# Performance work log

Hardware: AMD Instinct MI355X
Metric: run time of the kernel (lower is better)

Reference implementation:

```python
import jax, jax.numpy as jnp
import numpy as np

B, T, D, E, C = 4, 4096, 2048, 8, 1024
H = D // E  # per-expert hidden = out_features // num_experts = 256


def setup_inputs() -> dict:
    key = jax.random.key(0)
    ks = jax.random.split(key, 7)
    x = jax.random.normal(ks[0], (B, T, D), dtype=jnp.float32)
    # nn.Linear-style init scale ~ 1/sqrt(fan_in)
    W1 = jax.random.normal(ks[1], (E, H, D), dtype=jnp.float32) / np.sqrt(D)
    b1 = jax.random.normal(ks[2], (E, H), dtype=jnp.float32) / np.sqrt(D)
    W2 = jax.random.normal(ks[3], (E, D, H), dtype=jnp.float32) / np.sqrt(D)
    b2 = jax.random.normal(ks[4], (D,), dtype=jnp.float32) / np.sqrt(D)
    expert_indices = jax.random.randint(ks[5], (B, E, C), 0, T, dtype=jnp.int32)
    expert_gate = jax.random.uniform(ks[6], (B, E, C), dtype=jnp.float32)
    return {"x": x, "W1": W1, "b1": b1, "W2": W2, "b2": b2,
            "expert_indices": expert_indices, "expert_gate": expert_gate,
            "num_tokens": T}


def reference(x, W1, b1, W2, b2, expert_indices, expert_gate, num_tokens):
    # x: (B,T,D); expert_indices/expert_gate: (B,E,C)
    Bb = x.shape[0]
    Ee, Cc = expert_indices.shape[1], expert_indices.shape[2]
    b_idx = jnp.arange(Bb)[:, None, None]
    # dispatch: gather tokens per expert -> (B,E,C,D)
    sel = x[b_idx, expert_indices]
    # contract: per-expert GEMM -> (B,E,C,H)
    h = jnp.einsum('becd,ehd->bech', sel, W1) + b1[None, :, None, :]
    h = jax.nn.gelu(h, approximate=False)
    # expand: per-expert GEMM -> (B,E,C,D), shared output bias
    y = jnp.einsum('bech,eoh->beco', h, W2) + b2
    y = y * expert_gate[..., None]
    # combine: gated scatter-add back to token positions -> (B,T,D)
    out = jnp.zeros((Bb, num_tokens, x.shape[2]), dtype=x.dtype)
    out = out.at[jnp.arange(Bb)[:, None], expert_indices.reshape(Bb, Ee * Cc)].add(
        y.reshape(Bb, Ee * Cc, -1))
    return out
```

## Files before the change

### kernel.cpp

```cpp
#include <hip/hip_runtime.h>
#include <hip/hip_bf16.h>
#include <math.h>

#define B_ 4
#define T_ 4096
#define D_ 2048
#define E_ 8
#define C_ 1024
#define H_ 256
#define SLOTCAP 32

typedef unsigned short u16;
typedef unsigned long long u64;
typedef __attribute__((ext_vector_type(8))) short short8;
typedef __attribute__((ext_vector_type(4))) float f32x4;

__device__ __forceinline__ u16 f2bf_n(float f) {
    union { __hip_bfloat16 b; u16 u; } v;
    v.b = __float2bfloat16(f);
    return v.u;
}
__device__ __forceinline__ float bf2f(u16 u) {
    union { unsigned u; float f; } v; v.u = ((unsigned)u) << 16;
    return v.f;
}

__device__ __forceinline__ int swz(int row, int chunk) {
    return (row << 6) + ((chunk ^ (row & 7)) << 3);
}

__device__ __forceinline__ void gload16(const void* g, void* l) {
    __builtin_amdgcn_global_load_lds(
        (const __attribute__((address_space(1))) void*)g,
        (__attribute__((address_space(3))) void*)l, 16, 0, 0);
}

__global__ __launch_bounds__(256) void conv_x_bf16(
    const float* __restrict__ src, u16* __restrict__ dst, int n)
{
    int i = (blockIdx.x * 256 + threadIdx.x) * 4;
    if (i >= n) return;
    f32x4 v = *reinterpret_cast<const f32x4*>(src + i);
    u16 o[4];
    o[0] = f2bf_n(v[0]); o[1] = f2bf_n(v[1]); o[2] = f2bf_n(v[2]); o[3] = f2bf_n(v[3]);
    *reinterpret_cast<u64*>(dst + i) = *reinterpret_cast<const u64*>(o);
}

__global__ __launch_bounds__(256) void conv_w1_img(
    const float* __restrict__ W1, u16* __restrict__ img)
{
    const int cid = blockIdx.x * 256 + threadIdx.x;
    const int e = cid >> 16;
    const int kt = (cid >> 11) & 31;
    const int row = (cid >> 3) & 255;
    const int sc = cid & 7;
    const float* s = W1 + (((size_t)e * 256 + row) * 2048 + kt * 64
                           + ((sc ^ (row & 7)) << 3));
    f32x4 v0 = *reinterpret_cast<const f32x4*>(s);
    f32x4 v1 = *reinterpret_cast<const f32x4*>(s + 4);
    u16 o[8];
    #pragma unroll
    for (int j = 0; j < 4; ++j) { o[j] = f2bf_n(v0[j]); o[j + 4] = f2bf_n(v1[j]); }
    *reinterpret_cast<short8*>(img + (size_t)cid * 8) =
        *reinterpret_cast<const short8*>(o);
}

__global__ __launch_bounds__(256) void conv_w2_img(
    const float* __restrict__ W2, u16* __restrict__ img)
{
    const int cid = blockIdx.x * 256 + threadIdx.x;
    const int e = cid >> 16;
    const int nt = (cid >> 13) & 7;
    const int kt = (cid >> 11) & 3;
    const int row = (cid >> 3) & 255;
    const int sc = cid & 7;
    const float* s = W2 + (((size_t)e * 2048 + nt * 256 + row) * 256 + kt * 64
                           + ((sc ^ (row & 7)) << 3));
    f32x4 v0 = *reinterpret_cast<const f32x4*>(s);
    f32x4 v1 = *reinterpret_cast<const f32x4*>(s + 4);
    u16 o[8];
    #pragma unroll
    for (int j = 0; j < 4; ++j) { o[j] = f2bf_n(v0[j]); o[j + 4] = f2bf_n(v1[j]); }
    *reinterpret_cast<short8*>(img + (size_t)cid * 8) =
        *reinterpret_cast<const short8*>(o);
}

__global__ __launch_bounds__(512) void gemm1_v6(
    const u16* __restrict__ xbf, const u16* __restrict__ W1img,
    const float* __restrict__ b1, const int* __restrict__ idx,
    u16* __restrict__ Himg)
{
    const int mt = blockIdx.x;
    const int be = blockIdx.y;
    const int b = be >> 3, e = be & 7;
    const int m0 = mt * 128;

    __shared__ __align__(16) u16 As[2][8192];
    __shared__ __align__(16) u16 Bs[2][16384];
    __shared__ int toks[128];
    __shared__ float bs1[256];

    const int tid = threadIdx.x;
    if (tid < 128) toks[tid] = idx[(b * E_ + e) * C_ + m0 + tid];
    if (tid < 256) bs1[tid] = b1[e * H_ + tid];
    __syncthreads();

    const int lane = tid & 63, wid = tid >> 6;
    const int wm = wid >> 2, wn = wid & 3;
    const int l15 = lane & 15, lk = lane >> 4;

    const int s0 = tid;
    const int arow0 = s0 >> 3, asc = s0 & 7;
    const int arow1 = arow0 + 64;
    const u16* aSrc0 = xbf + ((size_t)b * T_ + toks[arow0]) * D_
                           + ((asc ^ (arow0 & 7)) << 3);
    const u16* aSrc1 = xbf + ((size_t)b * T_ + toks[arow1]) * D_
                           + ((asc ^ (arow1 & 7)) << 3);
    const u16* bSrc = W1img + (size_t)e * 32 * 16384 + (size_t)s0 * 8;
    const int ldsb = wid * 512;

#define G1_ISSUE(buf, kt)                                                     \
    do {                                                                      \
        const u16* b_ = bSrc + (size_t)(kt) * 16384;                          \
        gload16(aSrc0 + (kt) * 64, &As[buf][ldsb]);                           \
        gload16(aSrc1 + (kt) * 64, &As[buf][4096 + ldsb]);                    \
        gload16(b_,                &Bs[buf][ldsb]);                           \
        gload16(b_ + 4096,         &Bs[buf][4096 + ldsb]);                    \
        gload16(b_ + 8192,         &Bs[buf][8192 + ldsb]);                    \
        gload16(b_ + 12288,        &Bs[buf][12288 + ldsb]);                   \
    } while (0)

    f32x4 acc[4][4];
    #pragma unroll
    for (int i = 0; i < 4; ++i)
        #pragma unroll
        for (int j = 0; j < 4; ++j)
            acc[i][j] = (f32x4){0.f, 0.f, 0.f, 0.f};

    G1_ISSUE(0, 0);
    G1_ISSUE(1, 1);

    const int NT = D_ / 64;
    for (int t = 0; t < NT; ++t) {
        const int cur = t & 1;
        if (t < NT - 1) asm volatile("s_waitcnt vmcnt(6)" ::: "memory");
        else            asm volatile("s_waitcnt vmcnt(0)" ::: "memory");
        __builtin_amdgcn_s_barrier();
        __builtin_amdgcn_sched_barrier(0);
        #pragma unroll
        for (int kk = 0; kk < 2; ++kk) {
            short8 af[4], bfr[4];
            #pragma unroll
            for (int m = 0; m < 4; ++m) {
                const int row = wm * 64 + m * 16 + l15;
                af[m] = *reinterpret_cast<const short8*>(
                    &As[cur][swz(row, kk * 4 + lk)]);
            }
            #pragma unroll
            for (int n = 0; n < 4; ++n) {
                const int row = wn * 64 + n * 16 + l15;
                bfr[n] = *reinterpret_cast<const short8*>(
                    &Bs[cur][swz(row, kk * 4 + lk)]);
            }
            __builtin_amdgcn_s_setprio(1);
            #pragma unroll
            for (int m = 0; m < 4; ++m)
                #pragma unroll
                for (int n = 0; n < 4; ++n)
                    acc[m][n] = __builtin_amdgcn_mfma_f32_16x16x32_bf16(
                        bfr[n], af[m], acc[m][n], 0, 0, 0);
            __builtin_amdgcn_s_setprio(0);
        }
        asm volatile("s_waitcnt lgkmcnt(0)" ::: "memory");
        __builtin_amdgcn_s_barrier();
        __builtin_amdgcn_sched_barrier(0);
        if (t + 2 < NT) G1_ISSUE(cur, t + 2);
    }
#undef G1_ISSUE

    const size_t hblk = ((size_t)(be * 8 + mt) * 4 + wn) * 8192;
    #pragma unroll
    for (int m = 0; m < 4; ++m) {
        const int row = wm * 64 + m * 16 + l15;
        #pragma unroll
        for (int n = 0; n < 4; ++n) {
            const int hb = wn * 64 + n * 16 + lk * 4;
            u16 o[4];
            #pragma unroll
            for (int r = 0; r < 4; ++r) {
                float h = acc[m][n][r] + bs1[hb + r];
                float g = 0.5f * h * (1.0f + erff(h * 0.70710678118f));
                o[r] = f2bf_n(g);
            }
            const int lc = (n * 2 + (lk >> 1)) ^ (row & 7);
            u16* p = Himg + hblk + row * 64 + lc * 8 + (lk & 1) * 4;
            *reinterpret_cast<u64*>(p) = *reinterpret_cast<const u64*>(o);
        }
    }
}

__global__ __launch_bounds__(512) void gemm2_v4(
    const u16* __restrict__ Himg, const u16* __restrict__ W2img,
    const float* __restrict__ b2, const float* __restrict__ gate,
    u16* __restrict__ Ybuf)
{
    const int mt = blockIdx.x >> 3, nt = blockIdx.x & 7;
    const int be = blockIdx.y;
    const int b = be >> 3, e = be & 7;
    const int m0 = mt * 128, n0 = nt * 256;

    __shared__ __align__(16) u16 As[2][8192];
    __shared__ __align__(16) u16 Bs[2][16384];
    __shared__ float gs[128];
    __shared__ float bs2[256];

    const int tid = threadIdx.x;
    if (tid < 128) gs[tid] = gate[(b * E_ + e) * C_ + m0 + tid];
    if (tid < 256) bs2[tid] = b2[n0 + tid];
    __syncthreads();

    const int lane = tid & 63, wid = tid >> 6;
    const int wm = wid >> 2, wn = wid & 3;
    const int l15 = lane & 15, lk = lane >> 4;

    const int s0 = tid;
    const u16* aSrc = Himg + ((size_t)(be * 8 + mt) * 4) * 8192 + (size_t)s0 * 8;
    const u16* bSrc = W2img + ((size_t)(e * 8 + nt) * 4) * 16384 + (size_t)s0 * 8;
    const int ldsb = wid * 512;

#define G2_ISSUE(buf, kt)                                                     \
    do {                                                                      \
        const u16* a_ = aSrc + (size_t)(kt) * 8192;                           \
        const u16* b_ = bSrc + (size_t)(kt) * 16384;                          \
        gload16(a_,         &As[buf][ldsb]);                                  \
        gload16(a_ + 4096,  &As[buf][4096 + ldsb]);                           \
        gload16(b_,         &Bs[buf][ldsb]);                                  \
        gload16(b_ + 4096,  &Bs[buf][4096 + ldsb]);                           \
        gload16(b_ + 8192,  &Bs[buf][8192 + ldsb]);                           \
        gload16(b_ + 12288, &Bs[buf][12288 + ldsb]);                          \
    } while (0)

    f32x4 acc[4][4];
    #pragma unroll
    for (int i = 0; i < 4; ++i)
        #pragma unroll
        for (int j = 0; j < 4; ++j)
            acc[i][j] = (f32x4){0.f, 0.f, 0.f, 0.f};

    G2_ISSUE(0, 0);
    G2_ISSUE(1, 1);

    const int NT = H_ / 64;
    for (int t = 0; t < NT; ++t) {
        const int cur = t & 1;
        if (t < NT - 1) asm volatile("s_waitcnt vmcnt(6)" ::: "memory");
        else            asm volatile("s_waitcnt vmcnt(0)" ::: "memory");
        __builtin_amdgcn_s_barrier();
        __builtin_amdgcn_sched_barrier(0);
        #pragma unroll
        for (int kk = 0; kk < 2; ++kk) {
            short8 af[4], bfr[4];
            #pragma unroll
            for (int m = 0; m < 4; ++m) {
                const int row = wm * 64 + m * 16 + l15;
                af[m] = *reinterpret_cast<const short8*>(
                    &As[cur][swz(row, kk * 4 + lk)]);
            }
            #pragma unroll
            for (int n = 0; n < 4; ++n) {
                const int row = wn * 64 + n * 16 + l15;
                bfr[n] = *reinterpret_cast<const short8*>(
                    &Bs[cur][swz(row, kk * 4 + lk)]);
            }
            __builtin_amdgcn_s_setprio(1);
            #pragma unroll
            for (int m = 0; m < 4; ++m)
                #pragma unroll
                for (int n = 0; n < 4; ++n)
                    acc[m][n] = __builtin_amdgcn_mfma_f32_16x16x32_bf16(
                        bfr[n], af[m], acc[m][n], 0, 0, 0);
            __builtin_amdgcn_s_setprio(0);
        }
        asm volatile("s_waitcnt lgkmcnt(0)" ::: "memory");
        __builtin_amdgcn_s_barrier();
        __builtin_amdgcn_sched_barrier(0);
        if (t + 2 < NT) G2_ISSUE(cur, t + 2);
    }
#undef G2_ISSUE

    const size_t ybase = (size_t)(b * E_ + e) * C_ + m0;
    #pragma unroll
    for (int m = 0; m < 4; ++m) {
        const int cl = wm * 64 + m * 16 + l15;
        const float g = gs[cl];
        u16* rowp = Ybuf + (ybase + cl) * (size_t)D_ + n0;
        #pragma unroll
        for (int n = 0; n < 4; ++n) {
            const int db = wn * 64 + n * 16 + lk * 4;
            u16 o[4];
            #pragma unroll
            for (int r = 0; r < 4; ++r)
                o[r] = f2bf_n((acc[m][n][r] + bs2[db + r]) * g);
            *reinterpret_cast<u64*>(rowp + db) = *reinterpret_cast<const u64*>(o);
        }
    }
}

__global__ __launch_bounds__(256) void fill_kernel(
    const int* __restrict__ idx, int* __restrict__ cnt,
    int* __restrict__ slots)
{
    int i = blockIdx.x * 256 + threadIdx.x;
    if (i >= B_ * E_ * C_) return;
    int b = i / (E_ * C_);
    int slot = i % (E_ * C_);
    int t = idx[i];
    int p = atomicAdd(&cnt[b * T_ + t], 1);
    if (p < SLOTCAP) slots[(b * T_ + t) * SLOTCAP + p] = slot;
}

__global__ __launch_bounds__(256) void combine_kernel(
    const u16* __restrict__ Ybuf, const int* __restrict__ cnt,
    const int* __restrict__ slots, float* __restrict__ out)
{
    const int bt = blockIdx.x;
    const int tid = threadIdx.x;
    __shared__ int sl[SLOTCAP];
    int n = cnt[bt];
    n = n > SLOTCAP ? SLOTCAP : n;
    if (tid < n) sl[tid] = slots[bt * SLOTCAP + tid];
    __syncthreads();
    const int b = bt >> 12;
    float a[8] = {0.f, 0.f, 0.f, 0.f, 0.f, 0.f, 0.f, 0.f};
    for (int s = 0; s < n; ++s) {
        const u16* yrow = Ybuf + ((size_t)b * (E_ * C_) + sl[s]) * D_ + tid * 8;
        short8 v = *reinterpret_cast<const short8*>(yrow);
        #pragma unroll
        for (int j = 0; j < 8; ++j) a[j] += bf2f((u16)v[j]);
    }
    float* orow = out + (size_t)bt * D_ + tid * 8;
    *reinterpret_cast<f32x4*>(orow)     = (f32x4){a[0], a[1], a[2], a[3]};
    *reinterpret_cast<f32x4*>(orow + 4) = (f32x4){a[4], a[5], a[6], a[7]};
}

extern "C" void kernel_launch(void* const* d_in, const int* in_sizes, int n_in,
                              void* d_out, int out_size, void* d_ws, size_t ws_size,
                              hipStream_t stream) {
    const float* x    = (const float*)d_in[0];
    const float* W1   = (const float*)d_in[1];
    const float* b1   = (const float*)d_in[2];
    const float* W2   = (const float*)d_in[3];
    const float* b2   = (const float*)d_in[4];
    const int*   idx  = (const int*)d_in[5];
    const float* gate = (const float*)d_in[6];
    float* out = (float*)d_out;

    const size_t nW = (size_t)E_ * H_ * D_;
    const size_t nX = (size_t)B_ * T_ * D_;
    const size_t nH = (size_t)B_ * E_ * C_ * H_;
    const size_t nY = (size_t)B_ * E_ * C_ * D_;

    u16* W1img = (u16*)d_ws;
    u16* W2img = W1img + nW;
    u16* Himg  = W2img + nW;
    u16* Ybuf  = Himg + nH;
    u16* xbf   = Ybuf;
    int* cnt   = (int*)(Ybuf + nY);
    int* slots = cnt + (size_t)B_ * T_;

    hipMemsetAsync(cnt, 0, (size_t)B_ * T_ * sizeof(int), stream);
    conv_w1_img<<<2048, 256, 0, stream>>>(W1, W1img);
    conv_w2_img<<<2048, 256, 0, stream>>>(W2, W2img);
    conv_x_bf16<<<(int)(nX / 1024), 256, 0, stream>>>(x, xbf, (int)nX);
    fill_kernel<<<(B_ * E_ * C_) / 256, 256, 0, stream>>>(idx, cnt, slots);

    gemm1_v6<<<dim3(8, 32), 512, 0, stream>>>(xbf, W1img, b1, idx, Himg);
    gemm2_v4<<<dim3(64, 32), 512, 0, stream>>>(Himg, W2img, b2, gate, Ybuf);
    combine_kernel<<<B_ * T_, 256, 0, stream>>>(Ybuf, cnt, slots, out);
}
```

Before: 244.5 us.

## Replace double-buffered LDS pipeline with single-buffer synchronous loads in both GEMMs

Both expert GEMM kernels drop the two-stage LDS ping-pong prefetch and hand-tuned vmcnt waits. Each k-step now loads one tile into a single LDS buffer, calls __syncthreads, computes, then syncs again. This halves LDS use per block, which may let more blocks share a CU, especially for the 2048-block second GEMM. The cost is that global-load latency is no longer hidden behind MFMA work, which matters most for the 256-block first GEMM with its 32 k-steps.

```diff
diff --git a/kernel.cpp b/kernel.cpp
--- a/kernel.cpp
+++ b/kernel.cpp
@@ -85,7 +85,7 @@
         *reinterpret_cast<const short8*>(o);
 }
 
-__global__ __launch_bounds__(512) void gemm1_v6(
+__global__ __launch_bounds__(512) void gemm1_v7(
     const u16* __restrict__ xbf, const u16* __restrict__ W1img,
     const float* __restrict__ b1, const int* __restrict__ idx,
     u16* __restrict__ Himg)
@@ -95,8 +95,8 @@
     const int b = be >> 3, e = be & 7;
     const int m0 = mt * 128;
 
-    __shared__ __align__(16) u16 As[2][8192];
-    __shared__ __align__(16) u16 Bs[2][16384];
+    __shared__ __align__(16) u16 As[8192];
+    __shared__ __align__(16) u16 Bs[16384];
     __shared__ int toks[128];
     __shared__ float bs1[256];
 
@@ -119,17 +119,6 @@
     const u16* bSrc = W1img + (size_t)e * 32 * 16384 + (size_t)s0 * 8;
     const int ldsb = wid * 512;
 
-#define G1_ISSUE(buf, kt)                                                     \
-    do {                                                                      \
-        const u16* b_ = bSrc + (size_t)(kt) * 16384;                          \
-        gload16(aSrc0 + (kt) * 64, &As[buf][ldsb]);                           \
-        gload16(aSrc1 + (kt) * 64, &As[buf][4096 + ldsb]);                    \
-        gload16(b_,                &Bs[buf][ldsb]);                           \
-        gload16(b_ + 4096,         &Bs[buf][4096 + ldsb]);                    \
-        gload16(b_ + 8192,         &Bs[buf][8192 + ldsb]);                    \
-        gload16(b_ + 12288,        &Bs[buf][12288 + ldsb]);                   \
-    } while (0)
-
     f32x4 acc[4][4];
     #pragma unroll
     for (int i = 0; i < 4; ++i)
@@ -137,30 +126,30 @@
         for (int j = 0; j < 4; ++j)
             acc[i][j] = (f32x4){0.f, 0.f, 0.f, 0.f};
 
-    G1_ISSUE(0, 0);
-    G1_ISSUE(1, 1);
-
     const int NT = D_ / 64;
     for (int t = 0; t < NT; ++t) {
-        const int cur = t & 1;
-        if (t < NT - 1) asm volatile("s_waitcnt vmcnt(6)" ::: "memory");
-        else            asm volatile("s_waitcnt vmcnt(0)" ::: "memory");
-        __builtin_amdgcn_s_barrier();
-        __builtin_amdgcn_sched_barrier(0);
+        {
+            const u16* b_ = bSrc + (size_t)t * 16384;
+            gload16(aSrc0 + t * 64, &As[ldsb]);
+            gload16(aSrc1 + t * 64, &As[4096 + ldsb]);
+            gload16(b_,             &Bs[ldsb]);
+            gload16(b_ + 4096,      &Bs[4096 + ldsb]);
+            gload16(b_ + 8192,      &Bs[8192 + ldsb]);
+            gload16(b_ + 12288,     &Bs[12288 + ldsb]);
+        }
+        __syncthreads();
         #pragma unroll
         for (int kk = 0; kk < 2; ++kk) {
             short8 af[4], bfr[4];
             #pragma unroll
             for (int m = 0; m < 4; ++m) {
                 const int row = wm * 64 + m * 16 + l15;
-                af[m] = *reinterpret_cast<const short8*>(
-                    &As[cur][swz(row, kk * 4 + lk)]);
+                af[m] = *reinterpret_cast<const short8*>(&As[swz(row, kk * 4 + lk)]);
             }
             #pragma unroll
             for (int n = 0; n < 4; ++n) {
                 const int row = wn * 64 + n * 16 + l15;
-                bfr[n] = *reinterpret_cast<const short8*>(
-                    &Bs[cur][swz(row, kk * 4 + lk)]);
+                bfr[n] = *reinterpret_cast<const short8*>(&Bs[swz(row, kk * 4 + lk)]);
             }
             __builtin_amdgcn_s_setprio(1);
             #pragma unroll
@@ -171,12 +160,8 @@
                         bfr[n], af[m], acc[m][n], 0, 0, 0);
             __builtin_amdgcn_s_setprio(0);
         }
-        asm volatile("s_waitcnt lgkmcnt(0)" ::: "memory");
-        __builtin_amdgcn_s_barrier();
-        __builtin_amdgcn_sched_barrier(0);
-        if (t + 2 < NT) G1_ISSUE(cur, t + 2);
-    }
-#undef G1_ISSUE
+        __syncthreads();
+    }
 
     const size_t hblk = ((size_t)(be * 8 + mt) * 4 + wn) * 8192;
     #pragma unroll
@@ -199,7 +184,7 @@
     }
 }
 
-__global__ __launch_bounds__(512) void gemm2_v4(
+__global__ __launch_bounds__(512) void gemm2_v5(
     const u16* __restrict__ Himg, const u16* __restrict__ W2img,
     const float* __restrict__ b2, const float* __restrict__ gate,
     u16* __restrict__ Ybuf)
@@ -209,8 +194,8 @@
     const int b = be >> 3, e = be & 7;
     const int m0 = mt * 128, n0 = nt * 256;
 
-    __shared__ __align__(16) u16 As[2][8192];
-    __shared__ __align__(16) u16 Bs[2][16384];
+    __shared__ __align__(16) u16 As[8192];
+    __shared__ __align__(16) u16 Bs[16384];
     __shared__ float gs[128];
     __shared__ float bs2[256];
 
@@ -228,18 +213,6 @@
     const u16* bSrc = W2img + ((size_t)(e * 8 + nt) * 4) * 16384 + (size_t)s0 * 8;
     const int ldsb = wid * 512;
 
-#define G2_ISSUE(buf, kt)                                                     \
-    do {                                                                      \
-        const u16* a_ = aSrc + (size_t)(kt) * 8192;                           \
-        const u16* b_ = bSrc + (size_t)(kt) * 16384;                          \
-        gload16(a_,         &As[buf][ldsb]);                                  \
-        gload16(a_ + 4096,  &As[buf][4096 + ldsb]);                           \
-        gload16(b_,         &Bs[buf][ldsb]);                                  \
-        gload16(b_ + 4096,  &Bs[buf][4096 + ldsb]);                           \
-        gload16(b_ + 8192,  &Bs[buf][8192 + ldsb]);                           \
-        gload16(b_ + 12288, &Bs[buf][12288 + ldsb]);                          \
-    } while (0)
-
     f32x4 acc[4][4];
     #pragma unroll
     for (int i = 0; i < 4; ++i)
@@ -247,30 +220,31 @@
         for (int j = 0; j < 4; ++j)
             acc[i][j] = (f32x4){0.f, 0.f, 0.f, 0.f};
 
-    G2_ISSUE(0, 0);
-    G2_ISSUE(1, 1);
-
     const int NT = H_ / 64;
     for (int t = 0; t < NT; ++t) {
-        const int cur = t & 1;
-        if (t < NT - 1) asm volatile("s_waitcnt vmcnt(6)" ::: "memory");
-        else            asm volatile("s_waitcnt vmcnt(0)" ::: "memory");
-        __builtin_amdgcn_s_barrier();
-        __builtin_amdgcn_sched_barrier(0);
+        {
+            const u16* a_ = aSrc + (size_t)t * 8192;
+            const u16* b_ = bSrc + (size_t)t * 16384;
+            gload16(a_,         &As[ldsb]);
+            gload16(a_ + 4096,  &As[4096 + ldsb]);
+            gload16(b_,         &Bs[ldsb]);
+            gload16(b_ + 4096,  &Bs[4096 + ldsb]);
+            gload16(b_ + 8192,  &Bs[8192 + ldsb]);
+            gload16(b_ + 12288, &Bs[12288 + ldsb]);
+        }
+        __syncthreads();
         #pragma unroll
         for (int kk = 0; kk < 2; ++kk) {
             short8 af[4], bfr[4];
             #pragma unroll
             for (int m = 0; m < 4; ++m) {
                 const int row = wm * 64 + m * 16 + l15;
-                af[m] = *reinterpret_cast<const short8*>(
-                    &As[cur][swz(row, kk * 4 + lk)]);
+                af[m] = *reinterpret_cast<const short8*>(&As[swz(row, kk * 4 + lk)]);
             }
             #pragma unroll
             for (int n = 0; n < 4; ++n) {
                 const int row = wn * 64 + n * 16 + l15;
-                bfr[n] = *reinterpret_cast<const short8*>(
-                    &Bs[cur][swz(row, kk * 4 + lk)]);
+                bfr[n] = *reinterpret_cast<const short8*>(&Bs[swz(row, kk * 4 + lk)]);
             }
             __builtin_amdgcn_s_setprio(1);
             #pragma unroll
@@ -281,12 +255,8 @@
                         bfr[n], af[m], acc[m][n], 0, 0, 0);
             __builtin_amdgcn_s_setprio(0);
         }
-        asm volatile("s_waitcnt lgkmcnt(0)" ::: "memory");
-        __builtin_amdgcn_s_barrier();
-        __builtin_amdgcn_sched_barrier(0);
-        if (t + 2 < NT) G2_ISSUE(cur, t + 2);
-    }
-#undef G2_ISSUE
+        __syncthreads();
+    }
 
     const size_t ybase = (size_t)(b * E_ + e) * C_ + m0;
     #pragma unroll
@@ -374,7 +344,7 @@
     conv_x_bf16<<<(int)(nX / 1024), 256, 0, stream>>>(x, xbf, (int)nX);
     fill_kernel<<<(B_ * E_ * C_) / 256, 256, 0, stream>>>(idx, cnt, slots);
 
-    gemm1_v6<<<dim3(8, 32), 512, 0, stream>>>(xbf, W1img, b1, idx, Himg);
-    gemm2_v4<<<dim3(64, 32), 512, 0, stream>>>(Himg, W2img, b2, gate, Ybuf);
+    gemm1_v7<<<dim3(8, 32), 512, 0, stream>>>(xbf, W1img, b1, idx, Himg);
+    gemm2_v5<<<dim3(64, 32), 512, 0, stream>>>(Himg, W2img, b2, gate, Ybuf);
     combine_kernel<<<B_ * T_, 256, 0, stream>>>(Ybuf, cnt, slots, out);
 }
```

Measured after the change: 261.3 us. 6.9% more time.
